# Kernel optimization log

Measured on AMD Instinct MI355X. Metric: run time of the kernel, lower is better.

Reference implementation:

```python
import jax, jax.numpy as jnp
import numpy as np

B, L, D, H = 4, 4096, 2048, 16
HD = D // H  # head_dim = 128
EPS = 1e-9

def phi(x):
    # ELU(x) + 1 : non-negative feature map
    return jax.nn.elu(x) + 1.0

def setup_inputs() -> dict:
    key = jax.random.key(0)
    k1, k2, k3 = jax.random.split(key, 3)
    x = jax.random.normal(k1, (B, L, D), dtype=jnp.float32)
    W_qkv = jax.random.normal(k2, (3 * D, D), dtype=jnp.float32) * (D ** -0.5)
    W_out = jax.random.normal(k3, (D, D), dtype=jnp.float32) * (D ** -0.5)
    return {"x": x, "W_qkv": W_qkv, "W_out": W_out}

def reference(x, W_qkv, W_out):
    b, l, d = x.shape
    qkv = x @ W_qkv.T                      # (B, L, 3D)
    q, k, v = jnp.split(qkv, 3, axis=-1)   # each (B, L, D)
    # (B, L, H, HD) -> (B, H, L, HD)
    q = q.reshape(b, l, H, HD).transpose(0, 2, 1, 3)
    k = k.reshape(b, l, H, HD).transpose(0, 2, 1, 3)
    v = v.reshape(b, l, H, HD).transpose(0, 2, 1, 3)
    q = phi(q)
    k = phi(k)
    kv_cumsum = jnp.cumsum(k * v, axis=2)  # prefix sum over sequence dim
    k_cumsum = jnp.cumsum(k, axis=2)
    out = q * kv_cumsum / (q * k_cumsum + EPS)
    out = out.transpose(0, 2, 1, 3).reshape(b, l, d)
    return (out @ W_out.T) * (HD ** -0.5)
```

## Files before the change

kernel.cpp:

```cpp
#include <hip/hip_runtime.h>
#include <hip/hip_bf16.h>
#include <stdint.h>

#define B_ 4
#define L_ 4096
#define D_ 2048
#define TD_ (3 * D_)
#define CHUNKS 128
#define CLEN (L_ / CHUNKS)
#define M_ (B_ * L_)
#define K_ 2048
#define NT (K_ / 64)

typedef __bf16 bf16x8 __attribute__((ext_vector_type(8)));
typedef float f32x4 __attribute__((ext_vector_type(4)));
typedef ushort u16x8 __attribute__((ext_vector_type(8)));

__device__ __forceinline__ ushort f2bf(float f) {
  uint32_t u = __builtin_bit_cast(uint32_t, f);
  u += 0x7fffu + ((u >> 16) & 1u);
  return (ushort)(u >> 16);
}

__device__ __forceinline__ float bf2f(ushort u) {
  return __builtin_bit_cast(float, (uint32_t)u << 16);
}

__device__ __forceinline__ float phi_f(float x) {
  return x > 0.f ? x + 1.f : __expf(x);
}

__device__ __forceinline__ void gload_lds16(const ushort* g, ushort* l) {
  __builtin_amdgcn_global_load_lds(
      (__attribute__((address_space(1))) void*)(g),
      (__attribute__((address_space(3))) void*)(l), 16, 0, 0);
}

#define SBAR() __builtin_amdgcn_s_barrier()
#define SCHED0() __builtin_amdgcn_sched_barrier(0)
#define MFMA16(a, b, c) __builtin_amdgcn_mfma_f32_16x16x32_bf16((a), (b), (c), 0, 0, 0)

__global__ void cvt_bf16_kernel(const float* __restrict__ in,
                                ushort* __restrict__ out, int n4) {
  int i = blockIdx.x * blockDim.x + threadIdx.x;
  if (i >= n4) return;
  float4 v = reinterpret_cast<const float4*>(in)[i];
  ushort4 o;
  o.x = f2bf(v.x); o.y = f2bf(v.y); o.z = f2bf(v.z); o.w = f2bf(v.w);
  reinterpret_cast<ushort4*>(out)[i] = o;
}

__device__ __forceinline__ void stage8k(const ushort* __restrict__ G,
                                        int row0, int k0, char* lds8k,
                                        int tid) {
  const int p = tid * 16;
  const int row = tid >> 3;
  const int cb = (p & 127) ^ ((row & 7) << 4);
  gload_lds16(G + (size_t)(row0 + row) * K_ + k0 + (cb >> 1),
              (ushort*)(lds8k + p));
}

#define RD(p, off) (*reinterpret_cast<const bf16x8*>((p) + (off)))

#define KTILE(t, c)                                                            \
  {                                                                            \
                                                             \
    _Pragma("unroll") for (int i = 0; i < 4; ++i)                              \
        af1[i] = RD(bA1, (c) * 16384 + i * 2048);                              \
    _Pragma("unroll") for (int j = 0; j < 4; ++j)                              \
        bf1[j] = RD(bB1, (c) * 32768 + j * 2048);                              \
    if ((t) + 1 < NT) {                                                        \
      stage8k(A, rA, (t) * 64 + 64, lsA + (1 - (c)) * 16384, tid);             \
      stage8k(A, rA + 64, (t) * 64 + 64, lsA + (1 - (c)) * 16384 + 8192, tid); \
    }                                                                          \
    SCHED0();                                                                  \
    asm volatile("s_waitcnt lgkmcnt(8)" ::: "memory");                         \
    SCHED0();                                                                  \
    __builtin_amdgcn_s_setprio(1);                                             \
    _Pragma("unroll") for (int i = 0; i < 4; ++i)                              \
    _Pragma("unroll") for (int j = 0; j < 4; ++j)                              \
        acc[i][j] = MFMA16(af0[i], bf0[j], acc[i][j]);                         \
    __builtin_amdgcn_s_setprio(0);                                             \
                                                             \
    asm volatile("s_waitcnt lgkmcnt(0)" ::: "memory");                         \
    SCHED0();                                                                  \
    SBAR();                                                                    \
    if ((t) + 2 < NT) {                                                        \
      stage8k(Bm, rB, (t) * 64 + 128, lsB + (c) * 32768, tid);                 \
      stage8k(Bm, rB + 64, (t) * 64 + 128, lsB + (c) * 32768 + 8192, tid);     \
      stage8k(Bm, rB + 128, (t) * 64 + 128, lsB + (c) * 32768 + 16384, tid);   \
      stage8k(Bm, rB + 192, (t) * 64 + 128, lsB + (c) * 32768 + 24576, tid);   \
      SCHED0();                                                                \
      asm volatile("s_waitcnt vmcnt(4)" ::: "memory");                         \
    } else {                                                                   \
      SCHED0();                                                                \
      asm volatile("s_waitcnt vmcnt(0)" ::: "memory");                         \
    }                                                                          \
    SBAR();                                                                    \
    if ((t) + 1 < NT) {                                                        \
      _Pragma("unroll") for (int i = 0; i < 4; ++i)                            \
          af0[i] = RD(bA0, (1 - (c)) * 16384 + i * 2048);                      \
      _Pragma("unroll") for (int j = 0; j < 4; ++j)                            \
          bf0[j] = RD(bB0, (1 - (c)) * 32768 + j * 2048);                      \
    }                                                                          \
    SCHED0();                                                                  \
    __builtin_amdgcn_s_setprio(1);                                             \
    _Pragma("unroll") for (int i = 0; i < 4; ++i)                              \
    _Pragma("unroll") for (int j = 0; j < 4; ++j)                              \
        acc[i][j] = MFMA16(af1[i], bf1[j], acc[i][j]);                         \
    __builtin_amdgcn_s_setprio(0);                                             \
  }

__device__ __forceinline__ void gemm_core(const ushort* __restrict__ A,
                                          const ushort* __restrict__ Bm,
                                          int bm, int bn, char* ls,
                                          f32x4 (&acc)[4][4]) {
  const int tid = threadIdx.x;
  const int lane = tid & 63, wid = tid >> 6;
  const int wm = (wid >> 2) * 64, wn = (wid & 3) * 64;
  const int l16 = lane & 15, kg = lane >> 4;
  const int rA = bm * 128, rB = bn * 256;

  char* lsA = ls;
  char* lsB = ls + 32768;

  const int v16 = (l16 & 7) << 4;
  const int c0 = (kg * 16) ^ v16;
  const int c1 = (64 + kg * 16) ^ v16;
  const char* bA0 = lsA + (wm + l16) * 128 + c0;
  const char* bA1 = lsA + (wm + l16) * 128 + c1;
  const char* bB0 = lsB + (wn + l16) * 128 + c0;
  const char* bB1 = lsB + (wn + l16) * 128 + c1;

  stage8k(A, rA, 0, lsA, tid);
  stage8k(A, rA + 64, 0, lsA + 8192, tid);
  stage8k(Bm, rB, 0, lsB, tid);
  stage8k(Bm, rB + 64, 0, lsB + 8192, tid);
  stage8k(Bm, rB + 128, 0, lsB + 16384, tid);
  stage8k(Bm, rB + 192, 0, lsB + 24576, tid);
  stage8k(Bm, rB, 64, lsB + 32768, tid);
  stage8k(Bm, rB + 64, 64, lsB + 32768 + 8192, tid);
  stage8k(Bm, rB + 128, 64, lsB + 32768 + 16384, tid);
  stage8k(Bm, rB + 192, 64, lsB + 32768 + 24576, tid);
  asm volatile("s_waitcnt vmcnt(4)" ::: "memory");
  SBAR();

  bf16x8 af0[4], af1[4], bf0[4], bf1[4];
#pragma unroll
  for (int i = 0; i < 4; ++i) af0[i] = RD(bA0, i * 2048);
#pragma unroll
  for (int j = 0; j < 4; ++j) bf0[j] = RD(bB0, j * 2048);

#pragma unroll 1
  for (int t2 = 0; t2 < NT; t2 += 2) {
    KTILE(t2, 0);
    KTILE(t2 + 1, 1);
  }
}

__global__ __launch_bounds__(512, 2) void gemm_qkv8(
    const ushort* __restrict__ A, const ushort* __restrict__ Bm,
    ushort* __restrict__ qb, ushort* __restrict__ kb, ushort* __restrict__ vb) {
  extern __shared__ char ls[];
  const int nwg = gridDim.x;
  const int wg = blockIdx.x;
  const int swz = (wg & 7) * (nwg >> 3) + (wg >> 3);
  const int MT = M_ / 128;
  const int bm = swz % MT, bn = swz / MT;

  f32x4 acc[4][4] = {};
  gemm_core(A, Bm, bm, bn, ls, acc);

  const int seg = bn >> 3;
  ushort* dst = seg == 0 ? qb : (seg == 1 ? kb : vb);
  const int colbase = bn * 256 - seg * 2048;
  const int tid = threadIdx.x;
  const int lane = tid & 63, wid = tid >> 6;
  const int wm = (wid >> 2) * 64, wn = (wid & 3) * 64;
  const int l16 = lane & 15, kg = lane >> 4;
#pragma unroll
  for (int i = 0; i < 4; ++i) {
    const int row0 = bm * 128 + wm + i * 16 + kg * 4;
#pragma unroll
    for (int j = 0; j < 4; ++j) {
      const int col = colbase + wn + j * 16 + l16;
      ushort* cp = dst + (size_t)row0 * D_ + col;
#pragma unroll
      for (int r = 0; r < 4; ++r) cp[(size_t)r * D_] = f2bf(acc[i][j][r]);
    }
  }
}

__global__ __launch_bounds__(512, 2) void gemm_out8(
    const ushort* __restrict__ A, const ushort* __restrict__ Bm,
    float* __restrict__ C, float scale) {
  extern __shared__ char ls[];
  const int nwg = gridDim.x;
  const int wg = blockIdx.x;
  const int swz = (wg & 7) * (nwg >> 3) + (wg >> 3);
  const int MT = M_ / 128;
  const int bm = swz % MT, bn = swz / MT;

  f32x4 acc[4][4] = {};
  gemm_core(A, Bm, bm, bn, ls, acc);

  const int tid = threadIdx.x;
  const int lane = tid & 63, wid = tid >> 6;
  const int wm = (wid >> 2) * 64, wn = (wid & 3) * 64;
  const int l16 = lane & 15, kg = lane >> 4;
#pragma unroll
  for (int i = 0; i < 4; ++i) {
    const int row0 = bm * 128 + wm + i * 16 + kg * 4;
#pragma unroll
    for (int j = 0; j < 4; ++j) {
      const int col = bn * 256 + wn + j * 16 + l16;
      float* cp = C + (size_t)row0 * D_ + col;
#pragma unroll
      for (int r = 0; r < 4; ++r) cp[(size_t)r * D_] = acc[i][j][r] * scale;
    }
  }
}

__global__ void chunk_sums_kernel(const ushort* __restrict__ kb,
                                  const ushort* __restrict__ vb,
                                  float* __restrict__ sums) {
  const int d0 = threadIdx.x * 8;
  const int b = blockIdx.y, c = blockIdx.z;
  float sk[8] = {}, skv[8] = {};
  const size_t rowbase = (size_t)b * L_ + (size_t)c * CLEN;
  for (int l = 0; l < CLEN; ++l) {
    const size_t idx = (rowbase + l) * D_ + d0;
    u16x8 k8 = *reinterpret_cast<const u16x8*>(kb + idx);
    u16x8 v8 = *reinterpret_cast<const u16x8*>(vb + idx);
#pragma unroll
    for (int j = 0; j < 8; ++j) {
      float k = phi_f(bf2f(k8[j]));
      sk[j] += k;
      skv[j] = fmaf(k, bf2f(v8[j]), skv[j]);
    }
  }
  float* s = sums + ((size_t)(b * CHUNKS + c) * 2) * D_ + d0;
#pragma unroll
  for (int j = 0; j < 8; ++j) {
    s[j] = sk[j];
    s[D_ + j] = skv[j];
  }
}

__global__ void chunk_prefix_kernel(float* __restrict__ sums) {
  const int idx = blockIdx.x * 256 + threadIdx.x;
  const int b = idx >> 11, d = idx & (D_ - 1);
  float rk = 0.f, rkv = 0.f;
  for (int c = 0; c < CHUNKS; ++c) {
    float* s = sums + ((size_t)(b * CHUNKS + c) * 2) * D_ + d;
    float sk = s[0], skv = s[D_];
    s[0] = rk;
    s[D_] = rkv;
    rk += sk;
    rkv += skv;
  }
}

__global__ void apply_kernel(const ushort* __restrict__ qb,
                             const ushort* __restrict__ kb,
                             const ushort* __restrict__ vb,
                             const float* __restrict__ sums,
                             ushort* __restrict__ outb) {
  const int d0 = threadIdx.x * 8;
  const int b = blockIdx.y, c = blockIdx.z;
  const float* s = sums + ((size_t)(b * CHUNKS + c) * 2) * D_ + d0;
  float rk[8], rkv[8];
#pragma unroll
  for (int j = 0; j < 8; ++j) {
    rk[j] = s[j];
    rkv[j] = s[D_ + j];
  }
  const size_t rowbase = (size_t)b * L_ + (size_t)c * CLEN;
  for (int l = 0; l < CLEN; ++l) {
    const size_t idx = (rowbase + l) * D_ + d0;
    u16x8 q8 = *reinterpret_cast<const u16x8*>(qb + idx);
    u16x8 k8 = *reinterpret_cast<const u16x8*>(kb + idx);
    u16x8 v8 = *reinterpret_cast<const u16x8*>(vb + idx);
    u16x8 o8;
#pragma unroll
    for (int j = 0; j < 8; ++j) {
      float q = phi_f(bf2f(q8[j]));
      float k = phi_f(bf2f(k8[j]));
      float v = bf2f(v8[j]);
      rkv[j] = fmaf(k, v, rkv[j]);
      rk[j] += k;
      float o = (q * rkv[j]) / fmaf(q, rk[j], 1e-9f);
      o8[j] = f2bf(o);
    }
    *reinterpret_cast<u16x8*>(outb + idx) = o8;
  }
}

extern "C" void kernel_launch(void* const* d_in, const int* in_sizes, int n_in,
                              void* d_out, int out_size, void* d_ws, size_t ws_size,
                              hipStream_t stream) {
  (void)in_sizes; (void)n_in; (void)out_size; (void)ws_size;
  const float* x = (const float*)d_in[0];
  const float* Wqkv = (const float*)d_in[1];
  const float* Wout = (const float*)d_in[2];
  float* out = (float*)d_out;

  ushort* kb = (ushort*)d_out;
  ushort* vb = kb + (size_t)M_ * D_;

  char* ws = (char*)d_ws;
  size_t off = 0;
  auto alloc = [&](size_t bytes) -> void* {
    off = (off + 255) & ~(size_t)255;
    void* p = ws + off;
    off += bytes;
    return p;
  };
  ushort* qb = (ushort*)alloc((size_t)M_ * D_ * 2);
  ushort* xb = (ushort*)alloc((size_t)M_ * D_ * 2);
  ushort* wqb = (ushort*)alloc((size_t)TD_ * D_ * 2);
  ushort* wob = (ushort*)alloc((size_t)D_ * D_ * 2);
  float* sums = (float*)alloc((size_t)B_ * CHUNKS * 2 * D_ * 4);
  ushort* outb = xb;

  (void)hipFuncSetAttribute((const void*)gemm_qkv8,
                            hipFuncAttributeMaxDynamicSharedMemorySize, 98304);
  (void)hipFuncSetAttribute((const void*)gemm_out8,
                            hipFuncAttributeMaxDynamicSharedMemorySize, 98304);

  cvt_bf16_kernel<<<(M_ * D_ / 4 + 255) / 256, 256, 0, stream>>>(x, xb, M_ * D_ / 4);
  cvt_bf16_kernel<<<(TD_ * D_ / 4 + 255) / 256, 256, 0, stream>>>(Wqkv, wqb, TD_ * D_ / 4);
  cvt_bf16_kernel<<<(D_ * D_ / 4 + 255) / 256, 256, 0, stream>>>(Wout, wob, D_ * D_ / 4);

  gemm_qkv8<<<dim3((TD_ / 256) * (M_ / 128)), 512, 98304, stream>>>(xb, wqb, qb, kb, vb);

  chunk_sums_kernel<<<dim3(1, B_, CHUNKS), 256, 0, stream>>>(kb, vb, sums);
  chunk_prefix_kernel<<<dim3(B_ * D_ / 256), 256, 0, stream>>>(sums);
  apply_kernel<<<dim3(1, B_, CHUNKS), 256, 0, stream>>>(qb, kb, vb, sums, outb);

  gemm_out8<<<dim3((D_ / 256) * (M_ / 128)), 512, 98304, stream>>>(outb, wob, out,
                                                                   0.08838834764831845f);
}
```

Baseline: 664.8 us.

## Halve GEMM K-tile to 32 and shrink LDS to raise occupancy

The shared bf16 GEMM core now stages K in 32-wide tiles instead of 64, with a new XOR swizzle for 64-byte LDS rows. This halves dynamic LDS from 96KB to 48KB per block and raises launch bounds to allow 4 blocks per CU. The register double-buffering of A/B fragments is dropped in favour of a single fragment set with a barrier before each MFMA batch. The aim is better latency hiding through occupancy, at the cost of twice as many barriers per K step and less intra-wave overlap of LDS reads with MFMA.

```diff
diff --git a/kernel.cpp b/kernel.cpp
--- a/kernel.cpp
+++ b/kernel.cpp
@@ -10,7 +10,7 @@
 #define CLEN (L_ / CHUNKS)
 #define M_ (B_ * L_)
 #define K_ 2048
-#define NT (K_ / 64)
+#define NT (K_ / 32)
 
 typedef __bf16 bf16x8 __attribute__((ext_vector_type(8)));
 typedef float f32x4 __attribute__((ext_vector_type(4)));
@@ -38,6 +38,7 @@
 
 #define SBAR() __builtin_amdgcn_s_barrier()
 #define SCHED0() __builtin_amdgcn_sched_barrier(0)
+#define LGKM0() asm volatile("s_waitcnt lgkmcnt(0)" ::: "memory")
 #define MFMA16(a, b, c) __builtin_amdgcn_mfma_f32_16x16x32_bf16((a), (b), (c), 0, 0, 0)
 
 __global__ void cvt_bf16_kernel(const float* __restrict__ in,
@@ -50,13 +51,13 @@
   reinterpret_cast<ushort4*>(out)[i] = o;
 }
 
-__device__ __forceinline__ void stage8k(const ushort* __restrict__ G,
+__device__ __forceinline__ void stage32(const ushort* __restrict__ G,
                                         int row0, int k0, char* lds8k,
                                         int tid) {
   const int p = tid * 16;
-  const int row = tid >> 3;
-  const int cb = (p & 127) ^ ((row & 7) << 4);
-  gload_lds16(G + (size_t)(row0 + row) * K_ + k0 + (cb >> 1),
+  const int r = tid >> 2;
+  const int cb = (p & 63) ^ (((r >> 1) & 3) << 4);
+  gload_lds16(G + (size_t)(row0 + r) * K_ + k0 + (cb >> 1),
               (ushort*)(lds8k + p));
 }
 
@@ -64,51 +65,28 @@
 
 #define KTILE(t, c)                                                            \
   {                                                                            \
-                                                             \
     _Pragma("unroll") for (int i = 0; i < 4; ++i)                              \
-        af1[i] = RD(bA1, (c) * 16384 + i * 2048);                              \
+        af[i] = RD(bA, (c) * 8192 + i * 1024);                                 \
     _Pragma("unroll") for (int j = 0; j < 4; ++j)                              \
-        bf1[j] = RD(bB1, (c) * 32768 + j * 2048);                              \
-    if ((t) + 1 < NT) {                                                        \
-      stage8k(A, rA, (t) * 64 + 64, lsA + (1 - (c)) * 16384, tid);             \
-      stage8k(A, rA + 64, (t) * 64 + 64, lsA + (1 - (c)) * 16384 + 8192, tid); \
-    }                                                                          \
-    SCHED0();                                                                  \
-    asm volatile("s_waitcnt lgkmcnt(8)" ::: "memory");                         \
-    SCHED0();                                                                  \
+        bfr[j] = RD(bB, (c) * 16384 + j * 1024);                               \
+    if ((t) + 1 < NT)                                                          \
+      stage32(A, rA, ((t) + 1) * 32, lsA + (1 - (c)) * 8192, tid);             \
+    SCHED0(); SBAR(); LGKM0(); SCHED0();                                       \
     __builtin_amdgcn_s_setprio(1);                                             \
     _Pragma("unroll") for (int i = 0; i < 4; ++i)                              \
     _Pragma("unroll") for (int j = 0; j < 4; ++j)                              \
-        acc[i][j] = MFMA16(af0[i], bf0[j], acc[i][j]);                         \
+        acc[i][j] = MFMA16(af[i], bfr[j], acc[i][j]);                          \
     __builtin_amdgcn_s_setprio(0);                                             \
-                                                             \
-    asm volatile("s_waitcnt lgkmcnt(0)" ::: "memory");                         \
-    SCHED0();                                                                  \
-    SBAR();                                                                    \
     if ((t) + 2 < NT) {                                                        \
-      stage8k(Bm, rB, (t) * 64 + 128, lsB + (c) * 32768, tid);                 \
-      stage8k(Bm, rB + 64, (t) * 64 + 128, lsB + (c) * 32768 + 8192, tid);     \
-      stage8k(Bm, rB + 128, (t) * 64 + 128, lsB + (c) * 32768 + 16384, tid);   \
-      stage8k(Bm, rB + 192, (t) * 64 + 128, lsB + (c) * 32768 + 24576, tid);   \
+      stage32(Bm, rB, ((t) + 2) * 32, lsB + (c) * 16384, tid);                 \
+      stage32(Bm, rB + 128, ((t) + 2) * 32, lsB + (c) * 16384 + 8192, tid);    \
       SCHED0();                                                                \
-      asm volatile("s_waitcnt vmcnt(4)" ::: "memory");                         \
+      asm volatile("s_waitcnt vmcnt(2)" ::: "memory");                         \
     } else {                                                                   \
       SCHED0();                                                                \
       asm volatile("s_waitcnt vmcnt(0)" ::: "memory");                         \
     }                                                                          \
     SBAR();                                                                    \
-    if ((t) + 1 < NT) {                                                        \
-      _Pragma("unroll") for (int i = 0; i < 4; ++i)                            \
-          af0[i] = RD(bA0, (1 - (c)) * 16384 + i * 2048);                      \
-      _Pragma("unroll") for (int j = 0; j < 4; ++j)                            \
-          bf0[j] = RD(bB0, (1 - (c)) * 32768 + j * 2048);                      \
-    }                                                                          \
-    SCHED0();                                                                  \
-    __builtin_amdgcn_s_setprio(1);                                             \
-    _Pragma("unroll") for (int i = 0; i < 4; ++i)                              \
-    _Pragma("unroll") for (int j = 0; j < 4; ++j)                              \
-        acc[i][j] = MFMA16(af1[i], bf1[j], acc[i][j]);                         \
-    __builtin_amdgcn_s_setprio(0);                                             \
   }
 
 __device__ __forceinline__ void gemm_core(const ushort* __restrict__ A,
@@ -122,35 +100,21 @@
   const int rA = bm * 128, rB = bn * 256;
 
   char* lsA = ls;
-  char* lsB = ls + 32768;
-
-  const int v16 = (l16 & 7) << 4;
-  const int c0 = (kg * 16) ^ v16;
-  const int c1 = (64 + kg * 16) ^ v16;
-  const char* bA0 = lsA + (wm + l16) * 128 + c0;
-  const char* bA1 = lsA + (wm + l16) * 128 + c1;
-  const char* bB0 = lsB + (wn + l16) * 128 + c0;
-  const char* bB1 = lsB + (wn + l16) * 128 + c1;
-
-  stage8k(A, rA, 0, lsA, tid);
-  stage8k(A, rA + 64, 0, lsA + 8192, tid);
-  stage8k(Bm, rB, 0, lsB, tid);
-  stage8k(Bm, rB + 64, 0, lsB + 8192, tid);
-  stage8k(Bm, rB + 128, 0, lsB + 16384, tid);
-  stage8k(Bm, rB + 192, 0, lsB + 24576, tid);
-  stage8k(Bm, rB, 64, lsB + 32768, tid);
-  stage8k(Bm, rB + 64, 64, lsB + 32768 + 8192, tid);
-  stage8k(Bm, rB + 128, 64, lsB + 32768 + 16384, tid);
-  stage8k(Bm, rB + 192, 64, lsB + 32768 + 24576, tid);
-  asm volatile("s_waitcnt vmcnt(4)" ::: "memory");
+  char* lsB = ls + 16384;
+
+  const int cX = (kg * 16) ^ (((l16 >> 1) & 3) << 4);
+  const char* bA = lsA + (wm + l16) * 64 + cX;
+  const char* bB = lsB + (wn + l16) * 64 + cX;
+
+  stage32(A, rA, 0, lsA, tid);
+  stage32(Bm, rB, 0, lsB, tid);
+  stage32(Bm, rB + 128, 0, lsB + 8192, tid);
+  stage32(Bm, rB, 32, lsB + 16384, tid);
+  stage32(Bm, rB + 128, 32, lsB + 16384 + 8192, tid);
+  asm volatile("s_waitcnt vmcnt(2)" ::: "memory");
   SBAR();
 
-  bf16x8 af0[4], af1[4], bf0[4], bf1[4];
-#pragma unroll
-  for (int i = 0; i < 4; ++i) af0[i] = RD(bA0, i * 2048);
-#pragma unroll
-  for (int j = 0; j < 4; ++j) bf0[j] = RD(bB0, j * 2048);
-
+  bf16x8 af[4], bfr[4];
 #pragma unroll 1
   for (int t2 = 0; t2 < NT; t2 += 2) {
     KTILE(t2, 0);
@@ -158,7 +122,7 @@
   }
 }
 
-__global__ __launch_bounds__(512, 2) void gemm_qkv8(
+__global__ __launch_bounds__(512, 4) void gemm_qkv8(
     const ushort* __restrict__ A, const ushort* __restrict__ Bm,
     ushort* __restrict__ qb, ushort* __restrict__ kb, ushort* __restrict__ vb) {
   extern __shared__ char ls[];
@@ -191,7 +155,7 @@
   }
 }
 
-__global__ __launch_bounds__(512, 2) void gemm_out8(
+__global__ __launch_bounds__(512, 4) void gemm_out8(
     const ushort* __restrict__ A, const ushort* __restrict__ Bm,
     float* __restrict__ C, float scale) {
   extern __shared__ char ls[];
@@ -324,20 +288,20 @@
   ushort* outb = xb;
 
   (void)hipFuncSetAttribute((const void*)gemm_qkv8,
-                            hipFuncAttributeMaxDynamicSharedMemorySize, 98304);
+                            hipFuncAttributeMaxDynamicSharedMemorySize, 49152);
   (void)hipFuncSetAttribute((const void*)gemm_out8,
-                            hipFuncAttributeMaxDynamicSharedMemorySize, 98304);
+                            hipFuncAttributeMaxDynamicSharedMemorySize, 49152);
 
   cvt_bf16_kernel<<<(M_ * D_ / 4 + 255) / 256, 256, 0, stream>>>(x, xb, M_ * D_ / 4);
   cvt_bf16_kernel<<<(TD_ * D_ / 4 + 255) / 256, 256, 0, stream>>>(Wqkv, wqb, TD_ * D_ / 4);
   cvt_bf16_kernel<<<(D_ * D_ / 4 + 255) / 256, 256, 0, stream>>>(Wout, wob, D_ * D_ / 4);
 
-  gemm_qkv8<<<dim3((TD_ / 256) * (M_ / 128)), 512, 98304, stream>>>(xb, wqb, qb, kb, vb);
+  gemm_qkv8<<<dim3((TD_ / 256) * (M_ / 128)), 512, 49152, stream>>>(xb, wqb, qb, kb, vb);
 
   chunk_sums_kernel<<<dim3(1, B_, CHUNKS), 256, 0, stream>>>(kb, vb, sums);
   chunk_prefix_kernel<<<dim3(B_ * D_ / 256), 256, 0, stream>>>(sums);
   apply_kernel<<<dim3(1, B_, CHUNKS), 256, 0, stream>>>(qb, kb, vb, sums, outb);
 
-  gemm_out8<<<dim3((D_ / 256) * (M_ / 128)), 512, 98304, stream>>>(outb, wob, out,
+  gemm_out8<<<dim3((D_ / 256) * (M_ / 128)), 512, 49152, stream>>>(outb, wob, out,
                                                                    0.08838834764831845f);
 }
```

Result: slower. 697.6 us (+4.9%).
